# Kernel tuning notes

Measured on AMD Instinct MI355X. Metric: run time of the kernel, lower is better.

Reference implementation:

```python
import jax, jax.numpy as jnp
import numpy as np

B, T, K, H = 4, 2048, 1024, 16
D = K // H

def setup_inputs() -> dict:
    key = jax.random.key(0)
    kx, kq, kk, kv = jax.random.split(key, 4)
    s = 1.0 / np.sqrt(K)
    return {
        "x": jax.random.normal(kx, (B, T, K), dtype=jnp.float32),
        "Wq": jax.random.normal(kq, (K, K), dtype=jnp.float32) * s,
        "Wk": jax.random.normal(kk, (K, K), dtype=jnp.float32) * s,
        "Wv": jax.random.normal(kv, (K, K), dtype=jnp.float32) * s,
    }

def reference(x, Wq, Wk, Wv):
    b, t, k = x.shape
    h, d = H, K // H
    # projections -> (b, h, t, d)
    q = (x @ Wq.T).reshape(b, t, h, d).transpose(0, 2, 1, 3)
    ke = (x @ Wk.T).reshape(b, t, h, d).transpose(0, 2, 1, 3)
    v = (x @ Wv.T).reshape(b, t, h, d).transpose(0, 2, 1, 3)
    scale = d ** (-0.25)  # applied to both q and k, as in the original
    scores = jnp.einsum('bhqd,bhkd->bhqk', q * scale, ke * scale)
    causal = jnp.triu(jnp.ones((t, t), dtype=bool), k=1)
    scores = jnp.where(causal, -jnp.inf, scores)
    attn = jax.nn.softmax(scores, axis=-1)
    out = jnp.einsum('bhqk,bhkd->bhqd', attn, v)
    return out.transpose(0, 2, 1, 3).reshape(b, t, k)
```

## Files before the change

kernel.cpp:

```cpp
#include <hip/hip_runtime.h>
#include <hip/hip_bf16.h>
#include <math.h>

#define B_   4
#define T_   2048
#define KDIM 1024
#define H_   16
#define D_   64
#define BH_  (B_*H_)
#define M_   (B_*T_)
#define NKT  (KDIM/64)

typedef __bf16 bf16;
typedef __bf16 bf16x8 __attribute__((ext_vector_type(8)));
typedef __bf16 bf16x4 __attribute__((ext_vector_type(4)));
typedef float  f32x4  __attribute__((ext_vector_type(4)));
typedef float  f32x16 __attribute__((ext_vector_type(16)));
typedef unsigned int u32;
typedef u32 u32x4 __attribute__((ext_vector_type(4)));

static __device__ __forceinline__ f32x4 mfma16(bf16x8 a, bf16x8 b, f32x4 c) {
    return __builtin_amdgcn_mfma_f32_16x16x32_bf16(a, b, c, 0, 0, 0);
}
static __device__ __forceinline__ f32x16 mfma32(bf16x8 a, bf16x8 b, f32x16 c) {
    return __builtin_amdgcn_mfma_f32_32x32x16_bf16(a, b, c, 0, 0, 0);
}
static __device__ __forceinline__ float exp2_fast(float x) {
    float r; asm("v_exp_f32 %0, %1" : "=v"(r) : "v"(x)); return r;
}

__global__ void cvt_f32_to_bf16(const float* __restrict__ src, bf16* __restrict__ dst, int n4) {
    int i = blockIdx.x * blockDim.x + threadIdx.x;
    if (i >= n4) return;
    float4 v = reinterpret_cast<const float4*>(src)[i];
    bf16x4 o;
    o.x = (bf16)v.x; o.y = (bf16)v.y; o.z = (bf16)v.z; o.w = (bf16)v.w;
    reinterpret_cast<bf16x4*>(dst)[i] = o;
}

__global__ __launch_bounds__(512) void proj_gemm256(
    const bf16* __restrict__ xb, const bf16* __restrict__ Wflat,
    bf16* __restrict__ Qb, bf16* __restrict__ Kb, bf16* __restrict__ Vtb)
{
    __shared__ __align__(16) char As[2][256*64*2];
    __shared__ __align__(16) char Bs[2][128*64*2];

    const int tid  = threadIdx.x;
    const int wid  = tid >> 6;
    const int lane = tid & 63;
    const int l15  = lane & 15, l4 = lane >> 4;
    const int wavem = wid >> 1, waven = wid & 1;

    const int orig = blockIdx.x;
    const int xcd  = orig & 7;
    const int idx  = orig >> 3;
    const int mblk = xcd * 4 + (idx & 3);
    const int nblk = idx >> 2;
    const int row0 = mblk * 256, col0 = nblk * 128;

    const bf16* asrc[4];
#pragma unroll
    for (int q = 0; q < 4; ++q) {
        int c   = q*512 + tid;
        int rr  = c >> 3;
        int cb  = (c & 7) * 16;
        int cbs = cb ^ ((rr & 7) << 4);
        asrc[q] = xb + (size_t)(row0 + rr)*KDIM + (cbs >> 1);
    }
    const bf16* bsrc[2];
#pragma unroll
    for (int q = 0; q < 2; ++q) {
        int c   = q*512 + tid;
        int rr  = c >> 3;
        int cb  = (c & 7) * 16;
        int cbs = cb ^ ((rr & 7) << 4);
        bsrc[q] = Wflat + (size_t)(col0 + rr)*KDIM + (cbs >> 1);
    }

    auto stage = [&](int kt, int b) {
        const int k0 = kt * 64;
#pragma unroll
        for (int q = 0; q < 4; ++q) {
            char* la = As[b] + (q*512 + wid*64)*16;
            __builtin_amdgcn_global_load_lds(
                (const __attribute__((address_space(1))) void*)(asrc[q] + k0),
                (__attribute__((address_space(3))) void*)la, 16, 0, 0);
        }
#pragma unroll
        for (int q = 0; q < 2; ++q) {
            char* lb = Bs[b] + (q*512 + wid*64)*16;
            __builtin_amdgcn_global_load_lds(
                (const __attribute__((address_space(1))) void*)(bsrc[q] + k0),
                (__attribute__((address_space(3))) void*)lb, 16, 0, 0);
        }
    };

    f32x4 acc[4][4] = {};

    const int sw    = (l15 & 7) << 4;
    const int arow  = (wavem*64 + l15) * 128;
    const int brow  = (waven*64 + l15) * 128;

    auto compute = [&](int b) {
        const char* Ap = As[b];
        const char* Bp = Bs[b];
#pragma unroll
        for (int kk = 0; kk < 2; ++kk) {
            const int cbk = (kk*64 + l4*16) ^ sw;
            bf16x8 af[4], bfr[4];
#pragma unroll
            for (int m = 0; m < 4; ++m)
                af[m] = *reinterpret_cast<const bf16x8*>(Ap + arow + m*2048 + cbk);
#pragma unroll
            for (int n = 0; n < 4; ++n)
                bfr[n] = *reinterpret_cast<const bf16x8*>(Bp + brow + n*2048 + cbk);
            __builtin_amdgcn_s_setprio(1);
#pragma unroll
            for (int m = 0; m < 4; ++m)
#pragma unroll
                for (int n = 0; n < 4; ++n)
                    acc[m][n] = mfma16(af[m], bfr[n], acc[m][n]);
            __builtin_amdgcn_s_setprio(0);
        }
    };

    stage(0, 0);
    stage(1, 1);

    for (int t = 0; t < NKT - 1; ++t) {
        const int b = t & 1;
        asm volatile("s_waitcnt vmcnt(6)" ::: "memory");
        __builtin_amdgcn_sched_barrier(0);
        __builtin_amdgcn_s_barrier();
        __builtin_amdgcn_sched_barrier(0);
        compute(b);
        asm volatile("s_waitcnt lgkmcnt(0)" ::: "memory");
        __builtin_amdgcn_sched_barrier(0);
        __builtin_amdgcn_s_barrier();
        __builtin_amdgcn_sched_barrier(0);
        if (t < NKT - 2) stage(t + 2, b);
    }
    asm volatile("s_waitcnt vmcnt(0)" ::: "memory");
    __builtin_amdgcn_sched_barrier(0);
    __builtin_amdgcn_s_barrier();
    __builtin_amdgcn_sched_barrier(0);
    compute((NKT - 1) & 1);

#pragma unroll
    for (int m = 0; m < 4; ++m)
#pragma unroll
        for (int n = 0; n < 4; ++n)
#pragma unroll
            for (int r = 0; r < 4; ++r) {
                int gi = row0 + wavem*64 + m*16 + l4*4 + r;
                int gj = col0 + waven*64 + n*16 + l15;
                int wz  = gj >> 10;
                int gjw = gj & 1023;
                float v = acc[m][n][r];
                if (wz == 0) v *= 0.18033688011112042f;
                bf16 o = (bf16)v;
                int bb = gi >> 11, tt = gi & (T_-1);
                int hh = gjw >> 6, dd = gjw & (D_-1);
                size_t bh = (size_t)bb*H_ + hh;
                if (wz == 0)      Qb [(bh*T_ + tt)*D_ + dd] = o;
                else if (wz == 1) Kb [(bh*T_ + tt)*D_ + dd] = o;
                else              Vtb[(bh*D_ + dd)*T_ + tt] = o;
            }
}

__global__ __launch_bounds__(256) void flash_attn3(
    const bf16* __restrict__ Qb, const bf16* __restrict__ Kb,
    const bf16* __restrict__ Vtb, float* __restrict__ out)
{
    __shared__ __align__(16) char Ksm[8192];
    __shared__ __align__(16) char Vsm[8192];

    const int tid  = threadIdx.x;
    const int wid  = tid >> 6;
    const int lane = tid & 63;
    const int l31  = lane & 31;
    const int hi   = lane >> 5;

    const int orig = blockIdx.x;
    const int wg   = (orig & 7) * 128 + (orig >> 3);
    const int bh   = wg >> 4;
    const int qblk = (15 - (wg & 15)) * 128;
    const int q0   = qblk + wid * 32;
    const int q_abs = q0 + l31;

    const bf16* qp = Qb + ((size_t)bh*T_ + q_abs)*D_ + hi*8;
    bf16x8 qf[4];
#pragma unroll
    for (int j = 0; j < 4; ++j)
        qf[j] = *reinterpret_cast<const bf16x8*>(qp + j*16);

    const bf16* kbase = Kb  + (size_t)bh*T_*D_;
    const bf16* vbase = Vtb + (size_t)bh*D_*T_;

    f32x16 o0 = {}; f32x16 o1 = {};
    float lsum = 0.f;

    const int my_nt  = (q0 + 31) >> 6;
    const int blk_nt = qblk/64 + 1;
    const int tmaskb = q_abs - 4*hi;

    const int r0 = tid >> 3,          r1 = (tid + 256) >> 3;
    const int e0 = (tid & 7) * 8,     e1 = e0;
    const u32 lds0 = (u32)((r0*128 + e0*2) ^ ((r0 & 7) << 4));
    const u32 lds1 = (u32)((r1*128 + e1*2) ^ ((r1 & 7) << 4));

    u32x4 kr0, kr1, vr0, vr1;
    auto issue = [&](int nt) {
        kr0 = *reinterpret_cast<const u32x4*>(kbase + ((size_t)(nt*64 + r0))*D_ + e0);
        kr1 = *reinterpret_cast<const u32x4*>(kbase + ((size_t)(nt*64 + r1))*D_ + e1);
        vr0 = *reinterpret_cast<const u32x4*>(vbase + (size_t)r0*T_ + nt*64 + e0);
        vr1 = *reinterpret_cast<const u32x4*>(vbase + (size_t)r1*T_ + nt*64 + e1);
    };
    issue(0);

    auto subtile = [&](int s, int kvb_abs, bool maskit, bf16x8& pA, bf16x8& pB) {
        f32x16 sacc = {};
        const int row = s*32 + l31;
        const int swk = (row & 7) << 4;
#pragma unroll
        for (int j = 0; j < 4; ++j) {
            bf16x8 kf = *reinterpret_cast<const bf16x8*>(Ksm + ((row*128 + j*32 + hi*16) ^ swk));
            sacc = mfma32(kf, qf[j], sacc);
        }
        const int tlim = tmaskb - kvb_abs;
        float p[16];
#pragma unroll
        for (int r = 0; r < 16; ++r) {
            const int crow0 = (r & 3) + 8*(r >> 2);
            float sv = sacc[r];
            if (maskit) sv = (crow0 > tlim) ? -INFINITY : sv;
            p[r] = exp2_fast(sv);
        }
        {
            float a0 = p[0]+p[1],   a1 = p[2]+p[3],   a2 = p[4]+p[5],   a3 = p[6]+p[7];
            float a4 = p[8]+p[9],   a5 = p[10]+p[11], a6 = p[12]+p[13], a7 = p[14]+p[15];
            lsum += ((a0+a1) + (a2+a3)) + ((a4+a5) + (a6+a7));
        }
        u32 w[8];
#pragma unroll
        for (int i = 0; i < 8; ++i) {
            u32 wv;
            asm("v_cvt_pk_bf16_f32 %0, %1, %2" : "=v"(wv) : "v"(p[2*i]), "v"(p[2*i+1]));
            w[i] = wv;
        }
        u32 a0w = w[0], a2w = w[2];
        asm("v_permlane32_swap_b32 %0, %1" : "+v"(a0w), "+v"(a2w));
        u32 a1w = w[1], a3w = w[3];
        asm("v_permlane32_swap_b32 %0, %1" : "+v"(a1w), "+v"(a3w));
        u32 b0w = w[4], b2w = w[6];
        asm("v_permlane32_swap_b32 %0, %1" : "+v"(b0w), "+v"(b2w));
        u32 b1w = w[5], b3w = w[7];
        asm("v_permlane32_swap_b32 %0, %1" : "+v"(b1w), "+v"(b3w));
        u32x4 A0 = {a0w, a1w, a2w, a3w};
        u32x4 A1 = {b0w, b1w, b2w, b3w};
        pA = __builtin_bit_cast(bf16x8, A0);
        pB = __builtin_bit_cast(bf16x8, A1);
    };

    auto pv = [&](int ks, bf16x8 pf) {
        const int swv = (l31 & 7) << 4;
        const int colb = ks*32 + hi*16;
        bf16x8 v0 = *reinterpret_cast<const bf16x8*>(Vsm + ((l31*128 + colb) ^ swv));
        bf16x8 v1 = *reinterpret_cast<const bf16x8*>(Vsm + (((32 + l31)*128 + colb) ^ swv));
        o0 = mfma32(v0, pf, o0);
        o1 = mfma32(v1, pf, o1);
    };

    for (int nt = 0; nt <= blk_nt; ++nt) {
        __syncthreads();
        *reinterpret_cast<u32x4*>(Ksm + lds0) = kr0;
        *reinterpret_cast<u32x4*>(Ksm + lds1) = kr1;
        *reinterpret_cast<u32x4*>(Vsm + lds0) = vr0;
        *reinterpret_cast<u32x4*>(Vsm + lds1) = vr1;
        __syncthreads();
        if (nt < blk_nt) issue(nt + 1);

        if (nt <= my_nt) {
            const bool partial = (nt == my_nt);
            const int  nsub = (!partial || (q0 & 32)) ? 2 : 1;
            bf16x8 pA, pB;
            subtile(0, nt*64, partial, pA, pB);
            pv(0, pA);
            pv(1, pB);
            if (nsub == 2) {
                subtile(1, nt*64 + 32, partial, pA, pB);
                pv(2, pA);
                pv(3, pB);
            }
        }
    }

    lsum += __shfl_xor(lsum, 32);
    const float inv = 1.0f / lsum;
    const int bb = bh >> 4, hh = bh & 15;
    float* orow = out + ((size_t)bb*T_ + q_abs)*KDIM + hh*64 + hi*4;
#pragma unroll
    for (int g = 0; g < 4; ++g) {
        f32x4 v0, v1;
#pragma unroll
        for (int j = 0; j < 4; ++j) { v0[j] = o0[g*4+j]*inv; v1[j] = o1[g*4+j]*inv; }
        *reinterpret_cast<f32x4*>(orow + g*8)      = v0;
        *reinterpret_cast<f32x4*>(orow + 32 + g*8) = v1;
    }
}

extern "C" void kernel_launch(void* const* d_in, const int* in_sizes, int n_in,
                              void* d_out, int out_size, void* d_ws, size_t ws_size,
                              hipStream_t stream) {
    (void)in_sizes; (void)n_in; (void)out_size; (void)ws_size;
    const float* x  = (const float*)d_in[0];
    const float* Wq = (const float*)d_in[1];
    const float* Wk = (const float*)d_in[2];
    const float* Wv = (const float*)d_in[3];
    float* out = (float*)d_out;

    bf16* xb  = (bf16*)d_ws;
    bf16* Wb  = xb + (size_t)M_*KDIM;
    bf16* Qb  = Wb + (size_t)3*KDIM*KDIM;
    bf16* Kb  = Qb + (size_t)M_*KDIM;
    bf16* Vtb = Kb + (size_t)M_*KDIM;

    const int n4x = M_*KDIM/4;
    const int n4w = KDIM*KDIM/4;
    cvt_f32_to_bf16<<<(n4x+255)/256, 256, 0, stream>>>(x,  xb, n4x);
    cvt_f32_to_bf16<<<(n4w+255)/256, 256, 0, stream>>>(Wq, Wb,               n4w);
    cvt_f32_to_bf16<<<(n4w+255)/256, 256, 0, stream>>>(Wk, Wb + (size_t)KDIM*KDIM,   n4w);
    cvt_f32_to_bf16<<<(n4w+255)/256, 256, 0, stream>>>(Wv, Wb + (size_t)2*KDIM*KDIM, n4w);

    proj_gemm256<<<dim3(768), 512, 0, stream>>>(xb, Wb, Qb, Kb, Vtb);
    flash_attn3<<<dim3(BH_*16), 256, 0, stream>>>(Qb, Kb, Vtb, out);
}
```

Measured before the change: 167.7 us.

## Triple-buffer projection GEMM with one barrier per k-step; fuse conversion launches

The projection GEMM moves from a double-buffered LDS pipeline with two barriers per k-tile to a triple-buffered ring. The next-but-one tile is issued before computing the current one, so only one barrier per iteration is needed. The four f32-to-bf16 conversion launches are merged into one kernel writing the contiguous workspace, which removes launch overhead. LDS use grows from 96KB to 144KB per block, which may reduce occupancy or hit the LDS limit, and the fully unrolled loop raises code size.

```diff
diff --git a/kernel.cpp b/kernel.cpp
--- a/kernel.cpp
+++ b/kernel.cpp
@@ -29,10 +29,18 @@
     float r; asm("v_exp_f32 %0, %1" : "=v"(r) : "v"(x)); return r;
 }
 
-__global__ void cvt_f32_to_bf16(const float* __restrict__ src, bf16* __restrict__ dst, int n4) {
+__global__ void cvt_all(const float* __restrict__ x,  const float* __restrict__ Wq,
+                        const float* __restrict__ Wk, const float* __restrict__ Wv,
+                        bf16* __restrict__ dst) {
     int i = blockIdx.x * blockDim.x + threadIdx.x;
-    if (i >= n4) return;
-    float4 v = reinterpret_cast<const float4*>(src)[i];
+    const int NX = M_*KDIM/4, NW = KDIM*KDIM/4;
+    const float* src;
+    int j;
+    if (i < NX)                { src = x;  j = i; }
+    else if (i < NX + NW)      { src = Wq; j = i - NX; }
+    else if (i < NX + 2*NW)    { src = Wk; j = i - NX - NW; }
+    else                       { src = Wv; j = i - NX - 2*NW; }
+    float4 v = reinterpret_cast<const float4*>(src)[j];
     bf16x4 o;
     o.x = (bf16)v.x; o.y = (bf16)v.y; o.z = (bf16)v.z; o.w = (bf16)v.w;
     reinterpret_cast<bf16x4*>(dst)[i] = o;
@@ -42,8 +50,8 @@
     const bf16* __restrict__ xb, const bf16* __restrict__ Wflat,
     bf16* __restrict__ Qb, bf16* __restrict__ Kb, bf16* __restrict__ Vtb)
 {
-    __shared__ __align__(16) char As[2][256*64*2];
-    __shared__ __align__(16) char Bs[2][128*64*2];
+    __shared__ __align__(16) char As[3*32768];
+    __shared__ __align__(16) char Bs[3*16384];
 
     const int tid  = threadIdx.x;
     const int wid  = tid >> 6;
@@ -77,18 +85,20 @@
         bsrc[q] = Wflat + (size_t)(col0 + rr)*KDIM + (cbs >> 1);
     }
 
-    auto stage = [&](int kt, int b) {
+    auto stage = [&](int kt, int buf) {
         const int k0 = kt * 64;
+        char* Ab = As + buf*32768;
+        char* Bb = Bs + buf*16384;
 #pragma unroll
         for (int q = 0; q < 4; ++q) {
-            char* la = As[b] + (q*512 + wid*64)*16;
+            char* la = Ab + (q*512 + wid*64)*16;
             __builtin_amdgcn_global_load_lds(
                 (const __attribute__((address_space(1))) void*)(asrc[q] + k0),
                 (__attribute__((address_space(3))) void*)la, 16, 0, 0);
         }
 #pragma unroll
         for (int q = 0; q < 2; ++q) {
-            char* lb = Bs[b] + (q*512 + wid*64)*16;
+            char* lb = Bb + (q*512 + wid*64)*16;
             __builtin_amdgcn_global_load_lds(
                 (const __attribute__((address_space(1))) void*)(bsrc[q] + k0),
                 (__attribute__((address_space(3))) void*)lb, 16, 0, 0);
@@ -101,50 +111,51 @@
     const int arow  = (wavem*64 + l15) * 128;
     const int brow  = (waven*64 + l15) * 128;
 
-    auto compute = [&](int b) {
-        const char* Ap = As[b];
-        const char* Bp = Bs[b];
+    stage(0, 0);
+    stage(1, 1);
+    asm volatile("s_waitcnt vmcnt(6)" ::: "memory");
+    __builtin_amdgcn_sched_barrier(0);
+    __builtin_amdgcn_s_barrier();
+
+#pragma unroll
+    for (int t = 0; t < NKT; ++t) {
+        const int bt = t % 3;
+        const int b2 = (t + 2) % 3;
+        if (t + 2 < NKT) stage(t + 2, b2);
+
+        const char* Ap = As + bt*32768;
+        const char* Bp = Bs + bt*16384;
+        bf16x8 af[2][4], bfr[2][4];
 #pragma unroll
         for (int kk = 0; kk < 2; ++kk) {
             const int cbk = (kk*64 + l4*16) ^ sw;
-            bf16x8 af[4], bfr[4];
 #pragma unroll
             for (int m = 0; m < 4; ++m)
-                af[m] = *reinterpret_cast<const bf16x8*>(Ap + arow + m*2048 + cbk);
+                af[kk][m] = *reinterpret_cast<const bf16x8*>(Ap + arow + m*2048 + cbk);
 #pragma unroll
             for (int n = 0; n < 4; ++n)
-                bfr[n] = *reinterpret_cast<const bf16x8*>(Bp + brow + n*2048 + cbk);
-            __builtin_amdgcn_s_setprio(1);
+                bfr[kk][n] = *reinterpret_cast<const bf16x8*>(Bp + brow + n*2048 + cbk);
+        }
+        __builtin_amdgcn_s_setprio(1);
+#pragma unroll
+        for (int kk = 0; kk < 2; ++kk)
 #pragma unroll
             for (int m = 0; m < 4; ++m)
 #pragma unroll
                 for (int n = 0; n < 4; ++n)
-                    acc[m][n] = mfma16(af[m], bfr[n], acc[m][n]);
-            __builtin_amdgcn_s_setprio(0);
-        }
-    };
-
-    stage(0, 0);
-    stage(1, 1);
-
-    for (int t = 0; t < NKT - 1; ++t) {
-        const int b = t & 1;
-        asm volatile("s_waitcnt vmcnt(6)" ::: "memory");
-        __builtin_amdgcn_sched_barrier(0);
-        __builtin_amdgcn_s_barrier();
-        __builtin_amdgcn_sched_barrier(0);
-        compute(b);
-        asm volatile("s_waitcnt lgkmcnt(0)" ::: "memory");
-        __builtin_amdgcn_sched_barrier(0);
-        __builtin_amdgcn_s_barrier();
-        __builtin_amdgcn_sched_barrier(0);
-        if (t < NKT - 2) stage(t + 2, b);
-    }
-    asm volatile("s_waitcnt vmcnt(0)" ::: "memory");
-    __builtin_amdgcn_sched_barrier(0);
-    __builtin_amdgcn_s_barrier();
-    __builtin_amdgcn_sched_barrier(0);
-    compute((NKT - 1) & 1);
+                    acc[m][n] = mfma16(af[kk][m], bfr[kk][n], acc[m][n]);
+        __builtin_amdgcn_s_setprio(0);
+
+        if (t < NKT - 1) {
+            if (t + 2 < NKT) {
+                asm volatile("s_waitcnt vmcnt(6)" ::: "memory");
+            } else {
+                asm volatile("s_waitcnt vmcnt(0)" ::: "memory");
+            }
+            __builtin_amdgcn_sched_barrier(0);
+            __builtin_amdgcn_s_barrier();
+        }
+    }
 
 #pragma unroll
     for (int m = 0; m < 4; ++m)
@@ -325,12 +336,8 @@
     bf16* Kb  = Qb + (size_t)M_*KDIM;
     bf16* Vtb = Kb + (size_t)M_*KDIM;
 
-    const int n4x = M_*KDIM/4;
-    const int n4w = KDIM*KDIM/4;
-    cvt_f32_to_bf16<<<(n4x+255)/256, 256, 0, stream>>>(x,  xb, n4x);
-    cvt_f32_to_bf16<<<(n4w+255)/256, 256, 0, stream>>>(Wq, Wb,               n4w);
-    cvt_f32_to_bf16<<<(n4w+255)/256, 256, 0, stream>>>(Wk, Wb + (size_t)KDIM*KDIM,   n4w);
-    cvt_f32_to_bf16<<<(n4w+255)/256, 256, 0, stream>>>(Wv, Wb + (size_t)2*KDIM*KDIM, n4w);
+    const int n4 = (M_*KDIM + 3*KDIM*KDIM) / 4;
+    cvt_all<<<(n4 + 255)/256, 256, 0, stream>>>(x, Wq, Wk, Wv, xb);
 
     proj_gemm256<<<dim3(768), 512, 0, stream>>>(xb, Wb, Qb, Kb, Vtb);
     flash_attn3<<<dim3(BH_*16), 256, 0, stream>>>(Qb, Kb, Vtb, out);
```

After: 153.6 us. 8.4% less time.
